# Kernel optimization log

Measured on AMD Instinct MI355X. Metric: run time of the kernel, lower is better.

## Reference

```python
import jax, jax.numpy as jnp
import numpy as np

N, M, K = 500000, 8, 16


def setup_inputs() -> dict:
    key = jax.random.key(0)
    kp, kq, ka, kx = jax.random.split(key, 4)
    p = jax.random.normal(kp, (N, M), dtype=jnp.float32)
    q = jax.random.normal(kq, (N, M), dtype=jnp.float32)
    # scale transitions to be contractive so the length-N recurrence is stable
    a = 0.2 * jax.random.normal(ka, (N, M, M), dtype=jnp.float32)
    x = jax.random.normal(kx, (N, K), dtype=jnp.float32)
    return {"p": p, "q": q, "a": a, "x": x}


def reference(p, q, a, x):
    # StrictLowerTriQSM.matmul: y_i = p_i @ f_i, with recurrence
    # f_{i+1} = a_i @ f_i + outer(q_i, x_i), f_0 = 0.  f has shape (M, K).
    def impl(f, data):
        qi, ai, xi = data
        return ai @ f + jnp.outer(qi, xi), f

    init = jnp.zeros((M, x.shape[1]), dtype=x.dtype)
    _, f = jax.lax.scan(impl, init, (q, a, x))  # f: (N, M, K)
    return jnp.einsum("nm,nmk->nk", p, f)
```

## Files before the change

### kernel.cpp

```cpp
#include <hip/hip_runtime.h>


#define NTOT 500000

#define AS1(p) ((const __attribute__((address_space(1))) void*)(p))
#define AS3(p) ((__attribute__((address_space(3))) void*)(p))
#define GLOAD_LDS16(gp, lp) __builtin_amdgcn_global_load_lds(AS1(gp), AS3(lp), 16, 0, 0)
#define GLOAD_LDS4(gp, lp)  __builtin_amdgcn_global_load_lds(AS1(gp), AS3(lp), 4, 0, 0)
#define WAIT_VM(n) asm volatile("s_waitcnt vmcnt(" #n ")" ::: "memory")

static __device__ __forceinline__ int iminc(int a, int b) { return a < b ? a : b; }

template<int NC> struct P {
  static constexpr int CH   = (NC == 16384) ? 32 : 64;
  static constexpr int NST  = CH / 2;
  static constexpr int NG   = NC / 64;
  static constexpr int NS   = NG / 64;
  static constexpr int AGGA = 0;
  static constexpr int AGGB = NC * 64;
  static constexpr int GAGA = NC * 192;
  static constexpr int GAGB = NC * 192 + NG * 64;
  static constexpr int SGA  = NC * 192 + NG * 192;
  static constexpr int SGB  = NC * 192 + NG * 192 + NS * 64;
  static constexpr size_t BYTES = (size_t)(NC * 192 + NG * 192 + NS * 192) * 4u;
};

#define K1_COMP(E, VBS, VAS, VBD, VAD) do {                                  \
    const float xk_ = xgb[(E) * 32];                                         \
    const float4 q0_ = *(const float4*)(qgb + (E) * 8);                      \
    const float4 q1_ = *(const float4*)(qgb + (E) * 8 + 4);                  \
    const float qv_[8] = {q0_.x,q0_.y,q0_.z,q0_.w,q1_.x,q1_.y,q1_.z,q1_.w};  \
    _Pragma("unroll") for (int mm = 0; mm < 8; ++mm) {                       \
      const float4 r0_ = *(const float4*)(agb + (E) * 68 + mm * 8);          \
      const float4 r1_ = *(const float4*)(agb + (E) * 68 + mm * 8 + 4);      \
      VBD[mm] = qv_[mm] * xk_                                                \
              + r0_.x*VBS[0] + r0_.y*VBS[1] + r0_.z*VBS[2] + r0_.w*VBS[3]    \
              + r1_.x*VBS[4] + r1_.y*VBS[5] + r1_.z*VBS[6] + r1_.w*VBS[7];   \
      VAD[mm] = r0_.x*VAS[0] + r0_.y*VAS[1] + r0_.z*VAS[2] + r0_.w*VAS[3]    \
              + r1_.x*VAS[4] + r1_.y*VAS[5] + r1_.z*VAS[6] + r1_.w*VAS[7];   \
    }                                                                        \
  } while (0)

template<int NC>
__global__ __launch_bounds__(256, 4) void k1_aggregate(
    const float* __restrict__ q, const float* __restrict__ a,
    const float* __restrict__ x, float* __restrict__ ws)
{
  using PP = P<NC>;
  constexpr int CH = PP::CH, NST = PP::NST;
  __shared__ float sm[4 * 3 * 736];
  const int wv   = (int)(threadIdx.x >> 6);
  const int wave = blockIdx.x * 4 + wv;
  const int lane = (int)(threadIdx.x & 63);
  const int g    = lane >> 4;
  const int ll   = lane & 15;
  const int c    = wave * 4 + g;
  const bool hasA = ll >= 8;
  const int acol  = ll & 7;

  const int cb = wave * 4;
  float* b0 = sm + wv * 2208;
  float* b1 = b0 + 736;
  float* b2 = b0 + 1472;

  const int aoff = g * 136;
  const int qoff = 544 + g * 16;
  const int xoff = 608 + (g >> 1) * 64 + (g & 1) * 16 + ll;

  float vB0[8], vA0[8], vB1[8], vA1[8];
#pragma unroll
  for (int m = 0; m < 8; ++m) {
    vB0[m] = 0.f;
    vA0[m] = (hasA && m == acol) ? 1.f : 0.f;
  }

  auto stage = [&](int ss, float* lb) {
    const int base = cb * CH + ss * 2;
#pragma unroll
    for (int cc = 0; cc < 4; ++cc) {
#pragma unroll
      for (int e = 0; e < 2; ++e) {
        GLOAD_LDS4(a + (size_t)iminc(base + cc * CH + e, NTOT - 1) * 64u + lane,
                   lb + cc * 136 + e * 68);
      }
    }
    GLOAD_LDS4(q + (size_t)iminc(base + (lane >> 4) * CH + ((lane >> 3) & 1), NTOT - 1) * 8u + (lane & 7), lb + 544);
    GLOAD_LDS4(x + (size_t)iminc(base + ((lane >> 4) & 1) * CH + (lane >> 5), NTOT - 1) * 16u + (lane & 15), lb + 608);
    GLOAD_LDS4(x + (size_t)iminc(base + (2 + ((lane >> 4) & 1)) * CH + (lane >> 5), NTOT - 1) * 16u + (lane & 15), lb + 672);
  };

  stage(0, b0);
  stage(1, b1);
#pragma unroll 1
  for (int ss = 0; ss < NST; ++ss) {
    float* lb = b0;
    if (ss + 2 < NST) {
      stage(ss + 2, b2);
      WAIT_VM(22);
    } else if (ss + 1 < NST) {
      WAIT_VM(11);
    } else {
      WAIT_VM(0);
    }
    const float* agb = lb + aoff;
    const float* qgb = lb + qoff;
    const float* xgb = lb + xoff;
    K1_COMP(0, vB0, vA0, vB1, vA1);
    K1_COMP(1, vB1, vA1, vB0, vA0);
    float* t = b0; b0 = b1; b1 = b2; b2 = t;
  }

  {
    float* dst = ws + PP::AGGB + (size_t)c * 128u + (size_t)ll * 8u;
#pragma unroll
    for (int m = 0; m < 8; ++m) dst[m] = vB0[m];
  }
  if (hasA) {
    float* dst = ws + PP::AGGA + (size_t)c * 64u + (size_t)acol * 8u;
#pragma unroll
    for (int m = 0; m < 8; ++m) dst[m] = vA0[m];
  }
}

template<int NC, int LV>
__global__ __launch_bounds__(64) void k2scan(float* __restrict__ ws)
{
  using PP = P<NC>;
  constexpr int OFFAIN  = (LV == 0) ? PP::AGGA : PP::GAGA;
  constexpr int OFFBIN  = (LV == 0) ? PP::AGGB : PP::GAGB;
  constexpr int OFFAOUT = (LV == 0) ? PP::GAGA : PP::SGA;
  constexpr int OFFBOUT = (LV == 0) ? PP::GAGB : PP::SGB;
  __shared__ float sA[64 * 64];
  const int g    = blockIdx.x;
  const int lane = (int)(threadIdx.x & 63);
  const bool isB = lane < 16;
  const bool isA = (lane >= 16) && (lane < 24);
  const int bcol = lane & 15;
  const int acol = (lane - 16) & 7;

#pragma unroll 1
  for (int t = 0; t < 16; ++t)
    GLOAD_LDS16(ws + OFFAIN + (size_t)g * 4096u + t * 256 + lane * 4, sA + t * 256);

  float v[8];
#pragma unroll
  for (int m = 0; m < 8; ++m) v[m] = 0.f;
  if (isA) v[acol] = 1.f;

  float4 nb0, nb1;
  {
    const float* s = ws + OFFBIN + (size_t)(g * 64) * 128u + (size_t)bcol * 8u;
    nb0 = *(const float4*)s; nb1 = *(const float4*)(s + 4);
  }
  WAIT_VM(0);

#pragma unroll 1
  for (int j = 0; j < 64; ++j) {
    const int c = g * 64 + j;
    float bB[8] = {nb0.x, nb0.y, nb0.z, nb0.w, nb1.x, nb1.y, nb1.z, nb1.w};
    if (j + 1 < 64) {
      const float* s = ws + OFFBIN + (size_t)(c + 1) * 128u + (size_t)bcol * 8u;
      nb0 = *(const float4*)s; nb1 = *(const float4*)(s + 4);
    }
    if (isB) {
      float* dst = ws + OFFBIN + (size_t)c * 128u + (size_t)bcol * 8u;
#pragma unroll
      for (int m = 0; m < 8; ++m) dst[m] = v[m];
    } else if (isA) {
      float* dst = ws + OFFAIN + (size_t)c * 64u + (size_t)acol * 8u;
#pragma unroll
      for (int m = 0; m < 8; ++m) dst[m] = v[m];
    }
    const float* Aj = sA + j * 64;
    float nv[8];
#pragma unroll
    for (int m = 0; m < 8; ++m) nv[m] = 0.f;
#pragma unroll
    for (int t = 0; t < 8; ++t) {
      float4 col0 = *(const float4*)(Aj + t * 8);
      float4 col1 = *(const float4*)(Aj + t * 8 + 4);
      nv[0] += col0.x * v[t]; nv[1] += col0.y * v[t];
      nv[2] += col0.z * v[t]; nv[3] += col0.w * v[t];
      nv[4] += col1.x * v[t]; nv[5] += col1.y * v[t];
      nv[6] += col1.z * v[t]; nv[7] += col1.w * v[t];
    }
    if (isB) {
#pragma unroll
      for (int m = 0; m < 8; ++m) nv[m] += bB[m];
    }
#pragma unroll
    for (int m = 0; m < 8; ++m) v[m] = nv[m];
  }

  if (isB) {
    float* dst = ws + OFFBOUT + (size_t)g * 128u + (size_t)bcol * 8u;
#pragma unroll
    for (int m = 0; m < 8; ++m) dst[m] = v[m];
  } else if (isA) {
    float* dst = ws + OFFAOUT + (size_t)g * 64u + (size_t)acol * 8u;
#pragma unroll
    for (int m = 0; m < 8; ++m) dst[m] = v[m];
  }
}

template<int NC>
__global__ __launch_bounds__(64) void k2c_topscan(float* __restrict__ ws)
{
  using PP = P<NC>;
  const int lane = (int)(threadIdx.x & 63);
  const bool isB = lane < 16;
  const int bcol = lane & 15;

  float v[8];
#pragma unroll
  for (int m = 0; m < 8; ++m) v[m] = 0.f;

#pragma unroll 1
  for (int j = 0; j < PP::NS; ++j) {
    float bB[8];
    if (isB) {
      const float* s = ws + PP::SGB + (size_t)j * 128u + (size_t)bcol * 8u;
#pragma unroll
      for (int m = 0; m < 8; ++m) bB[m] = s[m];
      float* dst = ws + PP::SGB + (size_t)j * 128u + (size_t)bcol * 8u;
#pragma unroll
      for (int m = 0; m < 8; ++m) dst[m] = v[m];
    }
    const float* Aj = ws + PP::SGA + (size_t)j * 64u;
    float nv[8];
#pragma unroll
    for (int m = 0; m < 8; ++m) nv[m] = 0.f;
#pragma unroll
    for (int t = 0; t < 8; ++t) {
      float4 col0 = *(const float4*)(Aj + t * 8);
      float4 col1 = *(const float4*)(Aj + t * 8 + 4);
      nv[0] += col0.x * v[t]; nv[1] += col0.y * v[t];
      nv[2] += col0.z * v[t]; nv[3] += col0.w * v[t];
      nv[4] += col1.x * v[t]; nv[5] += col1.y * v[t];
      nv[6] += col1.z * v[t]; nv[7] += col1.w * v[t];
    }
    if (isB) {
#pragma unroll
      for (int m = 0; m < 8; ++m) nv[m] += bB[m];
    }
#pragma unroll
    for (int m = 0; m < 8; ++m) v[m] = nv[m];
  }
}

#define K3_COMP(E, FS, FD) do {                                              \
    const float xk_ = xgb[(E) * 32];                                         \
    const float4 q0_ = *(const float4*)(qgb + (E) * 8);                      \
    const float4 q1_ = *(const float4*)(qgb + (E) * 8 + 4);                  \
    const float4 p0_ = *(const float4*)(pgb + (E) * 8);                      \
    const float4 p1_ = *(const float4*)(pgb + (E) * 8 + 4);                  \
    const float y_ = p0_.x*FS[0] + p0_.y*FS[1] + p0_.z*FS[2] + p0_.w*FS[3]   \
                   + p1_.x*FS[4] + p1_.y*FS[5] + p1_.z*FS[6] + p1_.w*FS[7];  \
    const int i_ = c * CH + ss * 2 + (E);                                    \
    if (i_ < NTOT) out[(size_t)i_ * 16u + k] = y_;                           \
    const float qv_[8] = {q0_.x,q0_.y,q0_.z,q0_.w,q1_.x,q1_.y,q1_.z,q1_.w};  \
    _Pragma("unroll") for (int mm = 0; mm < 8; ++mm) {                       \
      const float4 r0_ = *(const float4*)(agb + (E) * 68 + mm * 8);          \
      const float4 r1_ = *(const float4*)(agb + (E) * 68 + mm * 8 + 4);      \
      FD[mm] = qv_[mm] * xk_                                                 \
             + r0_.x*FS[0] + r0_.y*FS[1] + r0_.z*FS[2] + r0_.w*FS[3]         \
             + r1_.x*FS[4] + r1_.y*FS[5] + r1_.z*FS[6] + r1_.w*FS[7];        \
    }                                                                        \
  } while (0)

template<int NC>
__global__ __launch_bounds__(256, 4) void k3_output(
    const float* __restrict__ p, const float* __restrict__ q,
    const float* __restrict__ a, const float* __restrict__ x,
    const float* __restrict__ ws, float* __restrict__ out)
{
  using PP = P<NC>;
  constexpr int CH = PP::CH, NST = PP::NST;
  __shared__ float sm3[4 * 3 * 800];
  const int wv   = (int)(threadIdx.x >> 6);
  const int wave = blockIdx.x * 4 + wv;
  const int lane = (int)(threadIdx.x & 63);
  const int g    = lane >> 4;
  const int k    = lane & 15;
  const int c    = wave * 4 + g;
  const int gr   = c >> 6;
  const int sidx = gr >> 6;

  const int cb = wave * 4;
  float* b0 = sm3 + wv * 2400;
  float* b1 = b0 + 800;
  float* b2 = b0 + 1600;

  const int aoff = g * 136;
  const int qoff = 544 + g * 16;
  const int poff = 608 + g * 16;
  const int xoff = 672 + (g >> 1) * 64 + (g & 1) * 16 + k;

  auto stage = [&](int ss, float* lb) {
    const int base = cb * CH + ss * 2;
#pragma unroll
    for (int cc = 0; cc < 4; ++cc) {
#pragma unroll
      for (int e = 0; e < 2; ++e) {
        GLOAD_LDS4(a + (size_t)iminc(base + cc * CH + e, NTOT - 1) * 64u + lane,
                   lb + cc * 136 + e * 68);
      }
    }
    GLOAD_LDS4(q + (size_t)iminc(base + (lane >> 4) * CH + ((lane >> 3) & 1), NTOT - 1) * 8u + (lane & 7), lb + 544);
    GLOAD_LDS4(p + (size_t)iminc(base + (lane >> 4) * CH + ((lane >> 3) & 1), NTOT - 1) * 8u + (lane & 7), lb + 608);
    GLOAD_LDS4(x + (size_t)iminc(base + ((lane >> 4) & 1) * CH + (lane >> 5), NTOT - 1) * 16u + (lane & 15), lb + 672);
    GLOAD_LDS4(x + (size_t)iminc(base + (2 + ((lane >> 4) & 1)) * CH + (lane >> 5), NTOT - 1) * 16u + (lane & 15), lb + 736);
  };

  stage(0, b0);
  stage(1, b1);

  const float* __restrict__ sBc = ws + PP::SGB  + (size_t)sidx * 128u + (size_t)k * 8u;
  const float* __restrict__ gBc = ws + PP::GAGB + (size_t)gr   * 128u + (size_t)k * 8u;
  const float* __restrict__ gA  = ws + PP::GAGA + (size_t)gr   * 64u;
  const float* __restrict__ pA  = ws + PP::AGGA + (size_t)c    * 64u;
  const float* __restrict__ lBc = ws + PP::AGGB + (size_t)c    * 128u + (size_t)k * 8u;
  float t1[8];
#pragma unroll
  for (int m = 0; m < 8; ++m) t1[m] = gBc[m];
#pragma unroll
  for (int t = 0; t < 8; ++t) {
    float4 c0 = *(const float4*)(gA + t * 8);
    float4 c1 = *(const float4*)(gA + t * 8 + 4);
    const float st = sBc[t];
    t1[0] += c0.x * st; t1[1] += c0.y * st; t1[2] += c0.z * st; t1[3] += c0.w * st;
    t1[4] += c1.x * st; t1[5] += c1.y * st; t1[6] += c1.z * st; t1[7] += c1.w * st;
  }
  float f0[8], f1[8];
#pragma unroll
  for (int m = 0; m < 8; ++m) f0[m] = lBc[m];
#pragma unroll
  for (int t = 0; t < 8; ++t) {
    float4 c0 = *(const float4*)(pA + t * 8);
    float4 c1 = *(const float4*)(pA + t * 8 + 4);
    const float gt = t1[t];
    f0[0] += c0.x * gt; f0[1] += c0.y * gt; f0[2] += c0.z * gt; f0[3] += c0.w * gt;
    f0[4] += c1.x * gt; f0[5] += c1.y * gt; f0[6] += c1.z * gt; f0[7] += c1.w * gt;
  }

#pragma unroll 1
  for (int ss = 0; ss < NST; ++ss) {
    float* lb = b0;
    if (ss + 2 < NST) {
      stage(ss + 2, b2);
      WAIT_VM(24);
    } else if (ss + 1 < NST) {
      WAIT_VM(12);
    } else {
      WAIT_VM(0);
    }
    const float* agb = lb + aoff;
    const float* qgb = lb + qoff;
    const float* pgb = lb + poff;
    const float* xgb = lb + xoff;
    K3_COMP(0, f0, f1);
    K3_COMP(1, f1, f0);
    float* t = b0; b0 = b1; b1 = b2; b2 = t;
  }
}

template<int NC>
static void launch_all(const float* p, const float* q, const float* a,
                       const float* x, float* out, float* ws, hipStream_t stream)
{
  using PP = P<NC>;
  hipLaunchKernelGGL(HIP_KERNEL_NAME(k1_aggregate<NC>), dim3(NC / 16), dim3(256), 0, stream, q, a, x, ws);
  hipLaunchKernelGGL(HIP_KERNEL_NAME(k2scan<NC, 0>),    dim3(PP::NG),  dim3(64),  0, stream, ws);
  hipLaunchKernelGGL(HIP_KERNEL_NAME(k2scan<NC, 1>),    dim3(PP::NS),  dim3(64),  0, stream, ws);
  hipLaunchKernelGGL(HIP_KERNEL_NAME(k2c_topscan<NC>),  dim3(1),       dim3(64),  0, stream, ws);
  hipLaunchKernelGGL(HIP_KERNEL_NAME(k3_output<NC>),    dim3(NC / 16), dim3(256), 0, stream, p, q, a, x, ws, out);
}

extern "C" void kernel_launch(void* const* d_in, const int* in_sizes, int n_in,
                              void* d_out, int out_size, void* d_ws, size_t ws_size,
                              hipStream_t stream)
{
  const float* p = (const float*)d_in[0];
  const float* q = (const float*)d_in[1];
  const float* a = (const float*)d_in[2];
  const float* x = (const float*)d_in[3];
  float* out = (float*)d_out;
  float* ws  = (float*)d_ws;

  if (ws_size >= P<16384>::BYTES) {
    launch_all<16384>(p, q, a, x, out, ws, stream);
  } else {
    launch_all<8192>(p, q, a, x, out, ws, stream);
  }
}
```

Before: 162.0 us.

## Remap lanes to 8 chunks per wave with two K columns per lane

Each lane now owns one row r of the chunk and carries two K columns (r and r+8) plus the A-aggregate column, so a wave processes 8 chunks instead of 4. Chunk count doubles (NC up to 32768, chunk length halved), staging loads one element per chunk per stage with incrementing pointers, and the pipeline loop is unrolled by two with explicit buffer rotation. The intent is more parallel chunks, better lane utilization (no idle A lanes), and cheaper address arithmetic, at the cost of more registers per lane and a larger scan workload in the k2 stages.

```diff
diff --git a/kernel.cpp b/kernel.cpp
--- a/kernel.cpp
+++ b/kernel.cpp
@@ -12,10 +12,10 @@
 static __device__ __forceinline__ int iminc(int a, int b) { return a < b ? a : b; }
 
 template<int NC> struct P {
-  static constexpr int CH   = (NC == 16384) ? 32 : 64;
-  static constexpr int NST  = CH / 2;
-  static constexpr int NG   = NC / 64;
-  static constexpr int NS   = NG / 64;
+  static constexpr int CH  = (NC == 32768) ? 16 : 32;
+  static constexpr int NST = CH;
+  static constexpr int NG  = NC / 64;
+  static constexpr int NS  = NG / 64;
   static constexpr int AGGA = 0;
   static constexpr int AGGB = NC * 64;
   static constexpr int GAGA = NC * 192;
@@ -25,19 +25,26 @@
   static constexpr size_t BYTES = (size_t)(NC * 192 + NG * 192 + NS * 192) * 4u;
 };
 
-#define K1_COMP(E, VBS, VAS, VBD, VAD) do {                                  \
-    const float xk_ = xgb[(E) * 32];                                         \
-    const float4 q0_ = *(const float4*)(qgb + (E) * 8);                      \
-    const float4 q1_ = *(const float4*)(qgb + (E) * 8 + 4);                  \
+#define K1_STEP(LB, SBa, SBb, SA, DBa, DBb, DA) do {                         \
+    const float* agb_ = (LB) + g68;                                          \
+    const float* qgb_ = (LB) + 544 + g8;                                     \
+    const float* xgb_ = (LB) + 608 + g16r;                                   \
+    const float xk0_ = xgb_[0], xk1_ = xgb_[8];                              \
+    const float4 q0_ = *(const float4*)(qgb_);                               \
+    const float4 q1_ = *(const float4*)(qgb_ + 4);                           \
     const float qv_[8] = {q0_.x,q0_.y,q0_.z,q0_.w,q1_.x,q1_.y,q1_.z,q1_.w};  \
     _Pragma("unroll") for (int mm = 0; mm < 8; ++mm) {                       \
-      const float4 r0_ = *(const float4*)(agb + (E) * 68 + mm * 8);          \
-      const float4 r1_ = *(const float4*)(agb + (E) * 68 + mm * 8 + 4);      \
-      VBD[mm] = qv_[mm] * xk_                                                \
-              + r0_.x*VBS[0] + r0_.y*VBS[1] + r0_.z*VBS[2] + r0_.w*VBS[3]    \
-              + r1_.x*VBS[4] + r1_.y*VBS[5] + r1_.z*VBS[6] + r1_.w*VBS[7];   \
-      VAD[mm] = r0_.x*VAS[0] + r0_.y*VAS[1] + r0_.z*VAS[2] + r0_.w*VAS[3]    \
-              + r1_.x*VAS[4] + r1_.y*VAS[5] + r1_.z*VAS[6] + r1_.w*VAS[7];   \
+      const float4 r0_ = *(const float4*)(agb_ + mm * 8);                    \
+      const float4 r1_ = *(const float4*)(agb_ + mm * 8 + 4);                \
+      DBa[mm] = qv_[mm] * xk0_                                               \
+        + r0_.x*SBa[0] + r0_.y*SBa[1] + r0_.z*SBa[2] + r0_.w*SBa[3]          \
+        + r1_.x*SBa[4] + r1_.y*SBa[5] + r1_.z*SBa[6] + r1_.w*SBa[7];         \
+      DBb[mm] = qv_[mm] * xk1_                                               \
+        + r0_.x*SBb[0] + r0_.y*SBb[1] + r0_.z*SBb[2] + r0_.w*SBb[3]          \
+        + r1_.x*SBb[4] + r1_.y*SBb[5] + r1_.z*SBb[6] + r1_.w*SBb[7];         \
+      DA[mm] =                                                               \
+          r0_.x*SA[0] + r0_.y*SA[1] + r0_.z*SA[2] + r0_.w*SA[3]              \
+        + r1_.x*SA[4] + r1_.y*SA[5] + r1_.z*SA[6] + r1_.w*SA[7];             \
     }                                                                        \
   } while (0)
 
@@ -47,78 +54,67 @@
     const float* __restrict__ x, float* __restrict__ ws)
 {
   using PP = P<NC>;
-  constexpr int CH = PP::CH, NST = PP::NST;
+  constexpr int CH = PP::CH, L = PP::NST / 2;
   __shared__ float sm[4 * 3 * 736];
   const int wv   = (int)(threadIdx.x >> 6);
   const int wave = blockIdx.x * 4 + wv;
   const int lane = (int)(threadIdx.x & 63);
-  const int g    = lane >> 4;
-  const int ll   = lane & 15;
-  const int c    = wave * 4 + g;
-  const bool hasA = ll >= 8;
-  const int acol  = ll & 7;
-
-  const int cb = wave * 4;
+  const int g    = lane >> 3;
+  const int r    = lane & 7;
+  const int c    = wave * 8 + g;
+
   float* b0 = sm + wv * 2208;
   float* b1 = b0 + 736;
   float* b2 = b0 + 1472;
 
-  const int aoff = g * 136;
-  const int qoff = 544 + g * 16;
-  const int xoff = 608 + (g >> 1) * 64 + (g & 1) * 16 + ll;
-
-  float vB0[8], vA0[8], vB1[8], vA1[8];
+  const int g68 = g * 68, g8 = g * 8, g16r = g * 16 + r;
+
+  const float* aBase[8];
+#pragma unroll
+  for (int cc = 0; cc < 8; ++cc)
+    aBase[cc] = a + (size_t)iminc((wave * 8 + cc) * CH, NTOT - CH) * 64u + lane;
+  const float* qPtr  = q + (size_t)iminc((wave * 8 + (lane >> 3)) * CH, NTOT - CH) * 8u + (lane & 7);
+  const float* xPtr0 = x + (size_t)iminc((wave * 8 + (lane >> 4)) * CH, NTOT - CH) * 16u + (lane & 15);
+  const float* xPtr1 = x + (size_t)iminc((wave * 8 + 4 + (lane >> 4)) * CH, NTOT - CH) * 16u + (lane & 15);
+  int soff = 0;
+
+  auto stage = [&](float* lb) {
+#pragma unroll
+    for (int cc = 0; cc < 8; ++cc)
+      GLOAD_LDS4(aBase[cc] + soff * 64, lb + cc * 68);
+    GLOAD_LDS4(qPtr, lb + 544);  qPtr  += 8;
+    GLOAD_LDS4(xPtr0, lb + 608); xPtr0 += 16;
+    GLOAD_LDS4(xPtr1, lb + 672); xPtr1 += 16;
+    ++soff;
+  };
+
+  float sBa[8], sBb[8], sAv[8], dBa[8], dBb[8], dAv[8];
 #pragma unroll
   for (int m = 0; m < 8; ++m) {
-    vB0[m] = 0.f;
-    vA0[m] = (hasA && m == acol) ? 1.f : 0.f;
-  }
-
-  auto stage = [&](int ss, float* lb) {
-    const int base = cb * CH + ss * 2;
-#pragma unroll
-    for (int cc = 0; cc < 4; ++cc) {
-#pragma unroll
-      for (int e = 0; e < 2; ++e) {
-        GLOAD_LDS4(a + (size_t)iminc(base + cc * CH + e, NTOT - 1) * 64u + lane,
-                   lb + cc * 136 + e * 68);
-      }
-    }
-    GLOAD_LDS4(q + (size_t)iminc(base + (lane >> 4) * CH + ((lane >> 3) & 1), NTOT - 1) * 8u + (lane & 7), lb + 544);
-    GLOAD_LDS4(x + (size_t)iminc(base + ((lane >> 4) & 1) * CH + (lane >> 5), NTOT - 1) * 16u + (lane & 15), lb + 608);
-    GLOAD_LDS4(x + (size_t)iminc(base + (2 + ((lane >> 4) & 1)) * CH + (lane >> 5), NTOT - 1) * 16u + (lane & 15), lb + 672);
-  };
-
-  stage(0, b0);
-  stage(1, b1);
+    sBa[m] = 0.f; sBb[m] = 0.f;
+    sAv[m] = (m == r) ? 1.f : 0.f;
+  }
+
+  stage(b0);
+  stage(b1);
 #pragma unroll 1
-  for (int ss = 0; ss < NST; ++ss) {
-    float* lb = b0;
-    if (ss + 2 < NST) {
-      stage(ss + 2, b2);
-      WAIT_VM(22);
-    } else if (ss + 1 < NST) {
-      WAIT_VM(11);
-    } else {
-      WAIT_VM(0);
-    }
-    const float* agb = lb + aoff;
-    const float* qgb = lb + qoff;
-    const float* xgb = lb + xoff;
-    K1_COMP(0, vB0, vA0, vB1, vA1);
-    K1_COMP(1, vB1, vA1, vB0, vA0);
-    float* t = b0; b0 = b1; b1 = b2; b2 = t;
+  for (int it = 0; it < L; ++it) {
+    if (it + 1 < L) { stage(b2); WAIT_VM(22); } else { WAIT_VM(11); }
+    K1_STEP(b0, sBa, sBb, sAv, dBa, dBb, dAv);
+    if (it + 1 < L) { stage(b0); WAIT_VM(22); } else { WAIT_VM(0); }
+    K1_STEP(b1, dBa, dBb, dAv, sBa, sBb, sAv);
+    float* t0 = b0; b0 = b2; b2 = b1; b1 = t0;
   }
 
   {
-    float* dst = ws + PP::AGGB + (size_t)c * 128u + (size_t)ll * 8u;
-#pragma unroll
-    for (int m = 0; m < 8; ++m) dst[m] = vB0[m];
-  }
-  if (hasA) {
-    float* dst = ws + PP::AGGA + (size_t)c * 64u + (size_t)acol * 8u;
-#pragma unroll
-    for (int m = 0; m < 8; ++m) dst[m] = vA0[m];
+    float* dB = ws + PP::AGGB + (size_t)c * 128u;
+#pragma unroll
+    for (int m = 0; m < 8; ++m) dB[r * 8 + m] = sBa[m];
+#pragma unroll
+    for (int m = 0; m < 8; ++m) dB[(r + 8) * 8 + m] = sBb[m];
+    float* dA = ws + PP::AGGA + (size_t)c * 64u + (size_t)r * 8u;
+#pragma unroll
+    for (int m = 0; m < 8; ++m) dA[m] = sAv[m];
   }
 }
 
@@ -248,24 +244,38 @@
   }
 }
 
-#define K3_COMP(E, FS, FD) do {                                              \
-    const float xk_ = xgb[(E) * 32];                                         \
-    const float4 q0_ = *(const float4*)(qgb + (E) * 8);                      \
-    const float4 q1_ = *(const float4*)(qgb + (E) * 8 + 4);                  \
-    const float4 p0_ = *(const float4*)(pgb + (E) * 8);                      \
-    const float4 p1_ = *(const float4*)(pgb + (E) * 8 + 4);                  \
-    const float y_ = p0_.x*FS[0] + p0_.y*FS[1] + p0_.z*FS[2] + p0_.w*FS[3]   \
-                   + p1_.x*FS[4] + p1_.y*FS[5] + p1_.z*FS[6] + p1_.w*FS[7];  \
-    const int i_ = c * CH + ss * 2 + (E);                                    \
-    if (i_ < NTOT) out[(size_t)i_ * 16u + k] = y_;                           \
+#define K3_STEP(LB, FSa, FSb, FDa, FDb) do {                                 \
+    const float* agb_ = (LB) + g68;                                          \
+    const float* qgb_ = (LB) + 544 + g8;                                     \
+    const float* pgb_ = (LB) + 608 + g8;                                     \
+    const float* xgb_ = (LB) + 672 + g16r;                                   \
+    const float xk0_ = xgb_[0], xk1_ = xgb_[8];                              \
+    const float4 q0_ = *(const float4*)(qgb_);                               \
+    const float4 q1_ = *(const float4*)(qgb_ + 4);                           \
+    const float4 p0_ = *(const float4*)(pgb_);                               \
+    const float4 p1_ = *(const float4*)(pgb_ + 4);                           \
+    const float ya_ = p0_.x*FSa[0] + p0_.y*FSa[1] + p0_.z*FSa[2]             \
+                    + p0_.w*FSa[3] + p1_.x*FSa[4] + p1_.y*FSa[5]             \
+                    + p1_.z*FSa[6] + p1_.w*FSa[7];                           \
+    const float yb_ = p0_.x*FSb[0] + p0_.y*FSb[1] + p0_.z*FSb[2]             \
+                    + p0_.w*FSb[3] + p1_.x*FSb[4] + p1_.y*FSb[5]             \
+                    + p1_.z*FSb[6] + p1_.w*FSb[7];                           \
+    if (ti < NTOT) {                                                         \
+      out[(size_t)ti * 16u + r] = ya_;                                       \
+      out[(size_t)ti * 16u + r + 8] = yb_;                                   \
+    }                                                                        \
     const float qv_[8] = {q0_.x,q0_.y,q0_.z,q0_.w,q1_.x,q1_.y,q1_.z,q1_.w};  \
     _Pragma("unroll") for (int mm = 0; mm < 8; ++mm) {                       \
-      const float4 r0_ = *(const float4*)(agb + (E) * 68 + mm * 8);          \
-      const float4 r1_ = *(const float4*)(agb + (E) * 68 + mm * 8 + 4);      \
-      FD[mm] = qv_[mm] * xk_                                                 \
-             + r0_.x*FS[0] + r0_.y*FS[1] + r0_.z*FS[2] + r0_.w*FS[3]         \
-             + r1_.x*FS[4] + r1_.y*FS[5] + r1_.z*FS[6] + r1_.w*FS[7];        \
+      const float4 r0_ = *(const float4*)(agb_ + mm * 8);                    \
+      const float4 r1_ = *(const float4*)(agb_ + mm * 8 + 4);                \
+      FDa[mm] = qv_[mm] * xk0_                                               \
+        + r0_.x*FSa[0] + r0_.y*FSa[1] + r0_.z*FSa[2] + r0_.w*FSa[3]          \
+        + r1_.x*FSa[4] + r1_.y*FSa[5] + r1_.z*FSa[6] + r1_.w*FSa[7];         \
+      FDb[mm] = qv_[mm] * xk1_                                               \
+        + r0_.x*FSb[0] + r0_.y*FSb[1] + r0_.z*FSb[2] + r0_.w*FSb[3]          \
+        + r1_.x*FSb[4] + r1_.y*FSb[5] + r1_.z*FSb[6] + r1_.w*FSb[7];         \
     }                                                                        \
+    ++ti;                                                                    \
   } while (0)
 
 template<int NC>
@@ -275,92 +285,88 @@
     const float* __restrict__ ws, float* __restrict__ out)
 {
   using PP = P<NC>;
-  constexpr int CH = PP::CH, NST = PP::NST;
+  constexpr int CH = PP::CH, L = PP::NST / 2;
   __shared__ float sm3[4 * 3 * 800];
   const int wv   = (int)(threadIdx.x >> 6);
   const int wave = blockIdx.x * 4 + wv;
   const int lane = (int)(threadIdx.x & 63);
-  const int g    = lane >> 4;
-  const int k    = lane & 15;
-  const int c    = wave * 4 + g;
+  const int g    = lane >> 3;
+  const int r    = lane & 7;
+  const int c    = wave * 8 + g;
   const int gr   = c >> 6;
-  const int sidx = gr >> 6;
-
-  const int cb = wave * 4;
+  const int si   = gr >> 6;
+
   float* b0 = sm3 + wv * 2400;
   float* b1 = b0 + 800;
   float* b2 = b0 + 1600;
 
-  const int aoff = g * 136;
-  const int qoff = 544 + g * 16;
-  const int poff = 608 + g * 16;
-  const int xoff = 672 + (g >> 1) * 64 + (g & 1) * 16 + k;
-
-  auto stage = [&](int ss, float* lb) {
-    const int base = cb * CH + ss * 2;
-#pragma unroll
-    for (int cc = 0; cc < 4; ++cc) {
-#pragma unroll
-      for (int e = 0; e < 2; ++e) {
-        GLOAD_LDS4(a + (size_t)iminc(base + cc * CH + e, NTOT - 1) * 64u + lane,
-                   lb + cc * 136 + e * 68);
-      }
-    }
-    GLOAD_LDS4(q + (size_t)iminc(base + (lane >> 4) * CH + ((lane >> 3) & 1), NTOT - 1) * 8u + (lane & 7), lb + 544);
-    GLOAD_LDS4(p + (size_t)iminc(base + (lane >> 4) * CH + ((lane >> 3) & 1), NTOT - 1) * 8u + (lane & 7), lb + 608);
-    GLOAD_LDS4(x + (size_t)iminc(base + ((lane >> 4) & 1) * CH + (lane >> 5), NTOT - 1) * 16u + (lane & 15), lb + 672);
-    GLOAD_LDS4(x + (size_t)iminc(base + (2 + ((lane >> 4) & 1)) * CH + (lane >> 5), NTOT - 1) * 16u + (lane & 15), lb + 736);
+  const int g68 = g * 68, g8 = g * 8, g16r = g * 16 + r;
+
+  const float* aBase[8];
+#pragma unroll
+  for (int cc = 0; cc < 8; ++cc)
+    aBase[cc] = a + (size_t)iminc((wave * 8 + cc) * CH, NTOT - CH) * 64u + lane;
+  const float* qPtr  = q + (size_t)iminc((wave * 8 + (lane >> 3)) * CH, NTOT - CH) * 8u + (lane & 7);
+  const float* pPtr  = p + (size_t)iminc((wave * 8 + (lane >> 3)) * CH, NTOT - CH) * 8u + (lane & 7);
+  const float* xPtr0 = x + (size_t)iminc((wave * 8 + (lane >> 4)) * CH, NTOT - CH) * 16u + (lane & 15);
+  const float* xPtr1 = x + (size_t)iminc((wave * 8 + 4 + (lane >> 4)) * CH, NTOT - CH) * 16u + (lane & 15);
+  int soff = 0;
+
+  auto stage = [&](float* lb) {
+#pragma unroll
+    for (int cc = 0; cc < 8; ++cc)
+      GLOAD_LDS4(aBase[cc] + soff * 64, lb + cc * 68);
+    GLOAD_LDS4(qPtr, lb + 544);  qPtr  += 8;
+    GLOAD_LDS4(pPtr, lb + 608);  pPtr  += 8;
+    GLOAD_LDS4(xPtr0, lb + 672); xPtr0 += 16;
+    GLOAD_LDS4(xPtr1, lb + 736); xPtr1 += 16;
+    ++soff;
   };
 
-  stage(0, b0);
-  stage(1, b1);
-
-  const float* __restrict__ sBc = ws + PP::SGB  + (size_t)sidx * 128u + (size_t)k * 8u;
-  const float* __restrict__ gBc = ws + PP::GAGB + (size_t)gr   * 128u + (size_t)k * 8u;
-  const float* __restrict__ gA  = ws + PP::GAGA + (size_t)gr   * 64u;
-  const float* __restrict__ pA  = ws + PP::AGGA + (size_t)c    * 64u;
-  const float* __restrict__ lBc = ws + PP::AGGB + (size_t)c    * 128u + (size_t)k * 8u;
-  float t1[8];
-#pragma unroll
-  for (int m = 0; m < 8; ++m) t1[m] = gBc[m];
+  stage(b0);
+  stage(b1);
+
+  const float* __restrict__ sB = ws + PP::SGB  + (size_t)si * 128u;
+  const float* __restrict__ gB = ws + PP::GAGB + (size_t)gr * 128u;
+  const float* __restrict__ gA = ws + PP::GAGA + (size_t)gr * 64u;
+  const float* __restrict__ pA = ws + PP::AGGA + (size_t)c  * 64u;
+  const float* __restrict__ lB = ws + PP::AGGB + (size_t)c  * 128u;
+  float t1a[8], t1b[8];
+#pragma unroll
+  for (int m = 0; m < 8; ++m) { t1a[m] = gB[r * 8 + m]; t1b[m] = gB[(r + 8) * 8 + m]; }
 #pragma unroll
   for (int t = 0; t < 8; ++t) {
     float4 c0 = *(const float4*)(gA + t * 8);
     float4 c1 = *(const float4*)(gA + t * 8 + 4);
-    const float st = sBc[t];
-    t1[0] += c0.x * st; t1[1] += c0.y * st; t1[2] += c0.z * st; t1[3] += c0.w * st;
-    t1[4] += c1.x * st; t1[5] += c1.y * st; t1[6] += c1.z * st; t1[7] += c1.w * st;
-  }
-  float f0[8], f1[8];
-#pragma unroll
-  for (int m = 0; m < 8; ++m) f0[m] = lBc[m];
+    const float sa = sB[r * 8 + t], sb = sB[(r + 8) * 8 + t];
+    t1a[0] += c0.x * sa; t1a[1] += c0.y * sa; t1a[2] += c0.z * sa; t1a[3] += c0.w * sa;
+    t1a[4] += c1.x * sa; t1a[5] += c1.y * sa; t1a[6] += c1.z * sa; t1a[7] += c1.w * sa;
+    t1b[0] += c0.x * sb; t1b[1] += c0.y * sb; t1b[2] += c0.z * sb; t1b[3] += c0.w * sb;
+    t1b[4] += c1.x * sb; t1b[5] += c1.y * sb; t1b[6] += c1.z * sb; t1b[7] += c1.w * sb;
+  }
+  float fa0[8], fb0[8], fa1[8], fb1[8];
+#pragma unroll
+  for (int m = 0; m < 8; ++m) { fa0[m] = lB[r * 8 + m]; fb0[m] = lB[(r + 8) * 8 + m]; }
 #pragma unroll
   for (int t = 0; t < 8; ++t) {
     float4 c0 = *(const float4*)(pA + t * 8);
     float4 c1 = *(const float4*)(pA + t * 8 + 4);
-    const float gt = t1[t];
-    f0[0] += c0.x * gt; f0[1] += c0.y * gt; f0[2] += c0.z * gt; f0[3] += c0.w * gt;
-    f0[4] += c1.x * gt; f0[5] += c1.y * gt; f0[6] += c1.z * gt; f0[7] += c1.w * gt;
-  }
+    const float ga = t1a[t], gb2 = t1b[t];
+    fa0[0] += c0.x * ga; fa0[1] += c0.y * ga; fa0[2] += c0.z * ga; fa0[3] += c0.w * ga;
+    fa0[4] += c1.x * ga; fa0[5] += c1.y * ga; fa0[6] += c1.z * ga; fa0[7] += c1.w * ga;
+    fb0[0] += c0.x * gb2; fb0[1] += c0.y * gb2; fb0[2] += c0.z * gb2; fb0[3] += c0.w * gb2;
+    fb0[4] += c1.x * gb2; fb0[5] += c1.y * gb2; fb0[6] += c1.z * gb2; fb0[7] += c1.w * gb2;
+  }
+
+  int ti = c * CH;
 
 #pragma unroll 1
-  for (int ss = 0; ss < NST; ++ss) {
-    float* lb = b0;
-    if (ss + 2 < NST) {
-      stage(ss + 2, b2);
-      WAIT_VM(24);
-    } else if (ss + 1 < NST) {
-      WAIT_VM(12);
-    } else {
-      WAIT_VM(0);
-    }
-    const float* agb = lb + aoff;
-    const float* qgb = lb + qoff;
-    const float* pgb = lb + poff;
-    const float* xgb = lb + xoff;
-    K3_COMP(0, f0, f1);
-    K3_COMP(1, f1, f0);
-    float* t = b0; b0 = b1; b1 = b2; b2 = t;
+  for (int it = 0; it < L; ++it) {
+    if (it + 1 < L) { stage(b2); WAIT_VM(24); } else { WAIT_VM(12); }
+    K3_STEP(b0, fa0, fb0, fa1, fb1);
+    if (it + 1 < L) { stage(b0); WAIT_VM(24); } else { WAIT_VM(0); }
+    K3_STEP(b1, fa1, fb1, fa0, fb0);
+    float* t0 = b0; b0 = b2; b2 = b1; b1 = t0;
   }
 }
 
@@ -369,11 +375,11 @@
                        const float* x, float* out, float* ws, hipStream_t stream)
 {
   using PP = P<NC>;
-  hipLaunchKernelGGL(HIP_KERNEL_NAME(k1_aggregate<NC>), dim3(NC / 16), dim3(256), 0, stream, q, a, x, ws);
+  hipLaunchKernelGGL(HIP_KERNEL_NAME(k1_aggregate<NC>), dim3(NC / 32), dim3(256), 0, stream, q, a, x, ws);
   hipLaunchKernelGGL(HIP_KERNEL_NAME(k2scan<NC, 0>),    dim3(PP::NG),  dim3(64),  0, stream, ws);
   hipLaunchKernelGGL(HIP_KERNEL_NAME(k2scan<NC, 1>),    dim3(PP::NS),  dim3(64),  0, stream, ws);
   hipLaunchKernelGGL(HIP_KERNEL_NAME(k2c_topscan<NC>),  dim3(1),       dim3(64),  0, stream, ws);
-  hipLaunchKernelGGL(HIP_KERNEL_NAME(k3_output<NC>),    dim3(NC / 16), dim3(256), 0, stream, p, q, a, x, ws, out);
+  hipLaunchKernelGGL(HIP_KERNEL_NAME(k3_output<NC>),    dim3(NC / 32), dim3(256), 0, stream, p, q, a, x, ws, out);
 }
 
 extern "C" void kernel_launch(void* const* d_in, const int* in_sizes, int n_in,
@@ -387,9 +393,9 @@
   float* out = (float*)d_out;
   float* ws  = (float*)d_ws;
 
-  if (ws_size >= P<16384>::BYTES) {
+  if (ws_size >= P<32768>::BYTES) {
+    launch_all<32768>(p, q, a, x, out, ws, stream);
+  } else {
     launch_all<16384>(p, q, a, x, out, ws, stream);
-  } else {
-    launch_all<8192>(p, q, a, x, out, ws, stream);
-  }
-}
+  }
+}
```

After: 177.6 us. +9.6%, slower.
